# Performance work log

Hardware: AMD Instinct MI355X
Metric: run time of the kernel (lower is better)

## Reference

```python
import jax, jax.numpy as jnp
import numpy as np

B, S, HD, HE = 32, 2048, 1024, 1024

def setup_inputs() -> dict:
    key = jax.random.key(0)
    k1, k2, k3, k4, k5, k6 = jax.random.split(key, 6)
    decoder_hidden = jax.random.normal(k1, (B, HD), dtype=jnp.float32)
    encoder_outputs = jax.random.normal(k2, (B, S, HE), dtype=jnp.float32)
    src_mask = jax.random.randint(k3, (B, S), 0, 2) > 0
    # nn.Linear weights stored as [out, in]; apply as x @ W.T
    s_q = 1.0 / np.sqrt(HD)
    s_k = 1.0 / np.sqrt(HE)
    W_query = jax.random.uniform(k4, (HD, HD), jnp.float32, -s_q, s_q)
    W_key = jax.random.uniform(k5, (HD, HE), jnp.float32, -s_k, s_k)
    W_energy = jax.random.uniform(k6, (1, HD), jnp.float32, -s_q, s_q)
    return {
        "decoder_hidden": decoder_hidden,
        "encoder_outputs": encoder_outputs,
        "src_mask": src_mask,
        "W_query": W_query,
        "W_key": W_key,
        "W_energy": W_energy,
    }

def reference(decoder_hidden, encoder_outputs, src_mask, W_query, W_key, W_energy):
    # q: [B, 1, HD], k: [B, S, HD]
    q = (decoder_hidden @ W_query.T)[:, None, :]
    k = jnp.einsum("bse,de->bsd", encoder_outputs, W_key)
    # scores: [B, S] = v^T tanh(q + k)
    scores = jnp.einsum("bsd,d->bs", jnp.tanh(q + k), W_energy[0])
    scores = jnp.where(src_mask, scores, -1e9)
    attn_weights = jax.nn.softmax(scores, axis=-1)
    context = jnp.einsum("bs,bse->be", attn_weights, encoder_outputs)
    return context, attn_weights
```

## Files before the change

### kernel.cpp

```cpp
#include <hip/hip_runtime.h>
#include <hip/hip_bf16.h>


#define NB 32
#define SS 2048
#define HD 1024
#define HE 1024
#define MM (NB * SS)
#define NT 32

typedef float f32x4 __attribute__((ext_vector_type(4)));
typedef short bf16x8 __attribute__((ext_vector_type(8)));
typedef short short4v __attribute__((ext_vector_type(4)));

static __device__ __forceinline__ short f2bf(float f) {
    union { __hip_bfloat16 h; short s; } u;
    u.h = __float2bfloat16(f);
    return u.s;
}
static __device__ __forceinline__ float bf2f(short s) {
    union { float f; unsigned u; } u;
    u.u = ((unsigned)(unsigned short)s) << 16;
    return u.f;
}

static __device__ __forceinline__ void gload16(const void* g, const void* l) {
    __builtin_amdgcn_global_load_lds(
        (const __attribute__((address_space(1))) void*)(uintptr_t)(g),
        (__attribute__((address_space(3))) void*)(unsigned)(uintptr_t)(l),
        16, 0, 0);
}

__global__ __launch_bounds__(256) void prep_kernel(const int* __restrict__ mask,
                                                   const float* __restrict__ dh,
                                                   const float* __restrict__ Wq,
                                                   const float* __restrict__ Wk,
                                                   int* __restrict__ idx,
                                                   int* __restrict__ cnt,
                                                   float* __restrict__ q,
                                                   short* __restrict__ wkb) {
    const int bid  = blockIdx.x;
    const int tid  = threadIdx.x;
    const int wid  = tid >> 6;
    const int lane = tid & 63;

    if (bid < 8) {
        const int b = bid * 4 + wid;
        int base = 0;
        for (int s0 = 0; s0 < SS; s0 += 64) {
            const int m = mask[b * SS + s0 + lane];
            const unsigned long long bal = __ballot(m != 0);
            const int rank = __popcll(bal & ((1ull << lane) - 1ull));
            if (m) idx[b * SS + base + rank] = s0 + lane;
            base += (int)__popcll(bal);
        }
        if (lane == 0) cnt[b] = base;
        for (int j = base + lane; j < SS; j += 64) idx[b * SS + j] = 0;
    } else if (bid < 264) {
        const int d = (bid - 8) * 4 + wid;
        const float* wrow = Wq + (long)d * HD + lane * 16;
        f32x4 w0 = *(const f32x4*)(wrow + 0);
        f32x4 w1 = *(const f32x4*)(wrow + 4);
        f32x4 w2 = *(const f32x4*)(wrow + 8);
        f32x4 w3 = *(const f32x4*)(wrow + 12);
        for (int b = 0; b < NB; ++b) {
            const float* drow = dh + b * HD + lane * 16;
            f32x4 d0 = *(const f32x4*)(drow + 0);
            f32x4 d1 = *(const f32x4*)(drow + 4);
            f32x4 d2 = *(const f32x4*)(drow + 8);
            f32x4 d3 = *(const f32x4*)(drow + 12);
            f32x4 s4 = w0 * d0 + w1 * d1 + w2 * d2 + w3 * d3;
            float dot = s4[0] + s4[1] + s4[2] + s4[3];
            #pragma unroll
            for (int off = 32; off > 0; off >>= 1)
                dot += __shfl_xor(dot, off, 64);
            if (lane == 0) q[b * HD + d] = dot;
        }
    } else {
        const int i = (bid - 264) * 256 + tid;
        const f32x4 a = *(const f32x4*)(Wk + (long)i * 8);
        const f32x4 b = *(const f32x4*)(Wk + (long)i * 8 + 4);
        bf16x8 o;
        o[0] = f2bf(a[0]); o[1] = f2bf(a[1]); o[2] = f2bf(a[2]); o[3] = f2bf(a[3]);
        o[4] = f2bf(b[0]); o[5] = f2bf(b[1]); o[6] = f2bf(b[2]); o[7] = f2bf(b[3]);
        *(bf16x8*)(wkb + (long)i * 8) = o;
    }
}

__global__ __launch_bounds__(256) void cvt_enc_kernel(const float* __restrict__ enc,
                                                      const int* __restrict__ idx,
                                                      const int* __restrict__ cnt,
                                                      short* __restrict__ encb) {
    const int b  = blockIdx.x >> 7;
    const int j0 = (blockIdx.x & 127) * 16;
    const int n  = cnt[b];
    const int nr = (n + 127) & ~127;
    if (j0 >= nr) return;
    const int j  = j0 + (threadIdx.x >> 4);
    const int c0 = (threadIdx.x & 15) * 8;
    short* dst = encb + ((long)b * SS + j) * HE + c0;
    if (j < n) {
        const float* src = enc + ((long)b * SS + idx[b * SS + j]) * HE + c0;
        #pragma unroll
        for (int u = 0; u < 8; ++u) {
            const f32x4 x = *(const f32x4*)(src + u * 128);
            const f32x4 y = *(const f32x4*)(src + u * 128 + 4);
            bf16x8 o;
            o[0] = f2bf(x[0]); o[1] = f2bf(x[1]); o[2] = f2bf(x[2]); o[3] = f2bf(x[3]);
            o[4] = f2bf(y[0]); o[5] = f2bf(y[1]); o[6] = f2bf(y[2]); o[7] = f2bf(y[3]);
            *(bf16x8*)(dst + u * 128) = o;
        }
    } else {
        const bf16x8 z = (bf16x8){0,0,0,0,0,0,0,0};
        #pragma unroll
        for (int u = 0; u < 8; ++u) *(bf16x8*)(dst + u * 128) = z;
    }
}

__global__ __launch_bounds__(256, 3) void score_mfma_kernel(const short* __restrict__ encb,
                                                            const short* __restrict__ wkb,
                                                            const float* __restrict__ qv,
                                                            const float* __restrict__ ven,
                                                            const int* __restrict__ cnt,
                                                            float* __restrict__ sp) {
    __shared__ __align__(16) short As[2][4096];
    __shared__ __align__(16) short Bs[2][4096];

    const int bid   = blockIdx.x;
    const int xcd   = bid & 7;
    const int slot  = bid >> 3;
    const int mtile = xcd * 64 + (slot >> 3);
    const int nt    = slot & 7;

    const int bb   = mtile >> 4;
    const int tile = mtile & 15;
    if (tile * 128 >= cnt[bb]) return;

    const int tid  = threadIdx.x;
    const int lane = tid & 63;
    const int wid  = tid >> 6;
    const int wr   = wid >> 1;
    const int wc   = wid & 1;
    const long mbase = (long)bb * SS + tile * 128;
    const int  nbase = nt * 128;

    f32x4 acc[4][4];
    #pragma unroll
    for (int m = 0; m < 4; ++m)
        #pragma unroll
        for (int n = 0; n < 4; ++n)
            acc[m][n] = (f32x4){0.f, 0.f, 0.f, 0.f};

    const short* ag0 = encb + (mbase + (tid >> 2)) * (long)HE + (tid & 3) * 8;
    const short* ag1 = ag0 + 64 * (long)HE;
    const short* bg0 = wkb + ((long)(nbase + (tid >> 2))) * HE + (tid & 3) * 8;
    const short* bg1 = bg0 + 64 * (long)HE;

    const int frow = lane & 15;
    const int kby  = (lane >> 4) * 16;

    #define COMPUTE(BUF)                                                         \
        do {                                                                     \
            bf16x8 af[4], bfr[4];                                                \
            _Pragma("unroll")                                                    \
            for (int m = 0; m < 4; ++m)                                          \
                af[m] = *(const bf16x8*)((const char*)As[BUF]                    \
                          + (wr * 64 + m * 16 + frow) * 64 + kby);               \
            _Pragma("unroll")                                                    \
            for (int n = 0; n < 4; ++n)                                          \
                bfr[n] = *(const bf16x8*)((const char*)Bs[BUF]                   \
                          + (wc * 64 + n * 16 + frow) * 64 + kby);               \
            _Pragma("unroll")                                                    \
            for (int m = 0; m < 4; ++m)                                          \
                _Pragma("unroll")                                                \
                for (int n = 0; n < 4; ++n)                                      \
                    acc[m][n] = __builtin_amdgcn_mfma_f32_16x16x32_bf16(         \
                        af[m], bfr[n], acc[m][n], 0, 0, 0);                      \
        } while (0)

    for (int kt = 0; kt < NT; kt += 2) {
        const int ko0 = kt * 32;
        const int ko1 = ko0 + 32;
        gload16(ag0 + ko0, (char*)As[0] + wid * 1024);
        gload16(ag1 + ko0, (char*)As[0] + 4096 + wid * 1024);
        gload16(bg0 + ko0, (char*)Bs[0] + wid * 1024);
        gload16(bg1 + ko0, (char*)Bs[0] + 4096 + wid * 1024);
        gload16(ag0 + ko1, (char*)As[1] + wid * 1024);
        gload16(ag1 + ko1, (char*)As[1] + 4096 + wid * 1024);
        gload16(bg0 + ko1, (char*)Bs[1] + wid * 1024);
        gload16(bg1 + ko1, (char*)Bs[1] + 4096 + wid * 1024);
        __syncthreads();
        COMPUTE(0);
        COMPUTE(1);
        __syncthreads();
    }
    #undef COMPUTE

    float qq[4], vv[4];
    #pragma unroll
    for (int n = 0; n < 4; ++n) {
        const int c = nbase + wc * 64 + n * 16 + frow;
        qq[n] = qv[bb * HD + c];
        vv[n] = ven[c];
    }
    float p[4][4];
    #pragma unroll
    for (int m = 0; m < 4; ++m) {
        #pragma unroll
        for (int rg = 0; rg < 4; ++rg) {
            float s = 0.f;
            #pragma unroll
            for (int n = 0; n < 4; ++n) {
                const float x = acc[m][n][rg] + qq[n];
                const float e = __expf(2.f * x);
                const float t = 1.f - 2.f * __builtin_amdgcn_rcpf(e + 1.f);
                s += vv[n] * t;
            }
            #pragma unroll
            for (int msk = 1; msk <= 8; msk <<= 1)
                s += __shfl_xor(s, msk, 64);
            p[m][rg] = s;
        }
    }
    if ((lane & 15) == 0) {
        const int g = lane >> 4;
        float* dst = sp + (long)(nt * 2 + wc) * MM;
        #pragma unroll
        for (int m = 0; m < 4; ++m)
            #pragma unroll
            for (int rg = 0; rg < 4; ++rg)
                dst[mbase + wr * 64 + m * 16 + g * 4 + rg] = p[m][rg];
    }
}

__global__ __launch_bounds__(256) void softmax_kernel(const float* __restrict__ sp,
                                                      const int* __restrict__ idx,
                                                      const int* __restrict__ cnt,
                                                      float* __restrict__ attn,
                                                      float* __restrict__ wcomp) {
    const int b = blockIdx.x;
    const int tid = threadIdx.x;
    const int lane = tid & 63;
    const int wid = tid >> 6;
    const int n = cnt[b];
    #pragma unroll
    for (int i = 0; i < 8; ++i)
        attn[b * SS + tid + i * 256] = 0.f;
    __shared__ float red[4];
    float sc[8];
    float mx = -3.0e38f;
    #pragma unroll
    for (int i = 0; i < 8; ++i) {
        const int j = tid + i * 256;
        float v = -3.0e38f;
        if (j < n) {
            v = 0.f;
            #pragma unroll
            for (int k = 0; k < 16; ++k)
                v += sp[(long)k * MM + b * SS + j];
        }
        sc[i] = v;
        mx = fmaxf(mx, v);
    }
    #pragma unroll
    for (int off = 32; off > 0; off >>= 1)
        mx = fmaxf(mx, __shfl_xor(mx, off, 64));
    if (lane == 0) red[wid] = mx;
    __syncthreads();
    mx = fmaxf(fmaxf(red[0], red[1]), fmaxf(red[2], red[3]));
    __syncthreads();
    float sum = 0.f;
    #pragma unroll
    for (int i = 0; i < 8; ++i) {
        const float e = (sc[i] > -1.0e38f) ? __expf(sc[i] - mx) : 0.f;
        sc[i] = e;
        sum += e;
    }
    #pragma unroll
    for (int off = 32; off > 0; off >>= 1)
        sum += __shfl_xor(sum, off, 64);
    if (lane == 0) red[wid] = sum;
    __syncthreads();
    sum = red[0] + red[1] + red[2] + red[3];
    const float inv = 1.f / sum;
    #pragma unroll
    for (int i = 0; i < 8; ++i) {
        const int j = tid + i * 256;
        const float w = sc[i] * inv;
        wcomp[b * SS + j] = w;
        if (j < n) attn[b * SS + idx[b * SS + j]] = w;
    }
}

__global__ __launch_bounds__(256) void ctx_partial_kernel(const short* __restrict__ encb,
                                                          const float* __restrict__ wcomp,
                                                          const int* __restrict__ cnt,
                                                          float* __restrict__ cp) {
    const int b = blockIdx.x >> 5;
    const int chunk = blockIdx.x & 31;
    const int tid = threadIdx.x;
    float* dst = cp + ((long)(b * 32 + chunk)) * HE + tid * 4;
    if (chunk * 64 >= cnt[b]) {
        *(f32x4*)dst = (f32x4){0.f, 0.f, 0.f, 0.f};
        return;
    }
    const short* ep = encb + ((long)b * SS + chunk * 64) * HE + tid * 4;
    const float* ap = wcomp + b * SS + chunk * 64;
    f32x4 acc = (f32x4){0.f, 0.f, 0.f, 0.f};
    #pragma unroll 4
    for (int s = 0; s < 64; ++s) {
        const float w = ap[s];
        const short4v v = *(const short4v*)(ep + (long)s * HE);
        acc[0] += w * bf2f(v[0]);
        acc[1] += w * bf2f(v[1]);
        acc[2] += w * bf2f(v[2]);
        acc[3] += w * bf2f(v[3]);
    }
    *(f32x4*)dst = acc;
}

__global__ __launch_bounds__(256) void ctx_reduce_kernel(const float* __restrict__ cp,
                                                         float* __restrict__ out) {
    const int o = blockIdx.x * 256 + threadIdx.x;
    const int b = o >> 10;
    const int e = o & 1023;
    float s = 0.f;
    #pragma unroll
    for (int c = 0; c < 32; ++c)
        s += cp[((long)(b * 32 + c)) * HE + e];
    out[o] = s;
}

extern "C" void kernel_launch(void* const* d_in, const int* in_sizes, int n_in,
                              void* d_out, int out_size, void* d_ws, size_t ws_size,
                              hipStream_t stream) {
    const float* dh   = (const float*)d_in[0];
    const float* enc  = (const float*)d_in[1];
    const int*   mask = (const int*)d_in[2];
    const float* Wq   = (const float*)d_in[3];
    const float* Wk   = (const float*)d_in[4];
    const float* Ve   = (const float*)d_in[5];

    float* out  = (float*)d_out;
    float* ctx  = out;
    float* attn = out + NB * HD;

    float* ws    = (float*)d_ws;
    float* wq_   = ws;
    float* sp    = ws + 32768;
    float* cp    = sp + 16 * (long)MM;
    short* wkb   = (short*)(cp + 32 * 32 * HE);
    float* wcomp = (float*)(wkb + (long)HD * HE);
    int*   idx   = (int*)(wcomp + MM);
    int*   cnt   = idx + MM;
    short* encb  = (short*)(cnt + 64);

    prep_kernel<<<776, 256, 0, stream>>>(mask, dh, Wq, Wk, idx, cnt, wq_, wkb);
    cvt_enc_kernel<<<NB * 128, 256, 0, stream>>>(enc, idx, cnt, encb);
    score_mfma_kernel<<<4096, 256, 0, stream>>>(encb, wkb, wq_, Ve, cnt, sp);
    softmax_kernel<<<NB, 256, 0, stream>>>(sp, idx, cnt, attn, wcomp);
    ctx_partial_kernel<<<1024, 256, 0, stream>>>(encb, wcomp, cnt, cp);
    ctx_reduce_kernel<<<128, 256, 0, stream>>>(cp, ctx);
}
```

Before: 164.2 us.

## Double-buffer score GEMM LDS stages to overlap global loads with MFMA

Doubles the LDS staging buffers so the next K-chunk is prefetched via direct-to-LDS loads while the current chunk is computed. Manual s_waitcnt vmcnt(8) plus barriers replace the two __syncthreads per iteration. The goal is to hide global memory latency behind MFMA work. In exchange, LDS usage doubles to 64KB per block and the occupancy hint drops from 3 to 2 blocks per CU, which could reduce latency hiding across blocks.

Result: slower. 169.2 us (+3.1%).

```diff
diff --git a/kernel.cpp b/kernel.cpp
--- a/kernel.cpp
+++ b/kernel.cpp
@@ -117,14 +117,14 @@
     }
 }
 
-__global__ __launch_bounds__(256, 3) void score_mfma_kernel(const short* __restrict__ encb,
+__global__ __launch_bounds__(256, 2) void score_mfma_kernel(const short* __restrict__ encb,
                                                             const short* __restrict__ wkb,
                                                             const float* __restrict__ qv,
                                                             const float* __restrict__ ven,
                                                             const int* __restrict__ cnt,
                                                             float* __restrict__ sp) {
-    __shared__ __align__(16) short As[2][4096];
-    __shared__ __align__(16) short Bs[2][4096];
+    __shared__ __align__(16) short As[4 * 4096];
+    __shared__ __align__(16) short Bs[4 * 4096];
 
     const int bid   = blockIdx.x;
     const int xcd   = bid & 7;
@@ -159,16 +159,33 @@
     const int frow = lane & 15;
     const int kby  = (lane >> 4) * 16;
 
-    #define COMPUTE(BUF)                                                         \
+    #define ABASE(BUF, T) ((char*)As + ((BUF) * 2 + (T)) * 8192)
+    #define BBASE(BUF, T) ((char*)Bs + ((BUF) * 2 + (T)) * 8192)
+
+    #define STAGE(BUF, E)                                            \
+        do {                                                         \
+            const int ko0_ = (E) * 64;                               \
+            const int ko1_ = ko0_ + 32;                              \
+            gload16(ag0 + ko0_, ABASE(BUF, 0) + wid * 1024);         \
+            gload16(ag1 + ko0_, ABASE(BUF, 0) + 4096 + wid * 1024);  \
+            gload16(bg0 + ko0_, BBASE(BUF, 0) + wid * 1024);         \
+            gload16(bg1 + ko0_, BBASE(BUF, 0) + 4096 + wid * 1024);  \
+            gload16(ag0 + ko1_, ABASE(BUF, 1) + wid * 1024);         \
+            gload16(ag1 + ko1_, ABASE(BUF, 1) + 4096 + wid * 1024);  \
+            gload16(bg0 + ko1_, BBASE(BUF, 1) + wid * 1024);         \
+            gload16(bg1 + ko1_, BBASE(BUF, 1) + 4096 + wid * 1024);  \
+        } while (0)
+
+    #define COMPUTE(BUF, T)                                                      \
         do {                                                                     \
             bf16x8 af[4], bfr[4];                                                \
             _Pragma("unroll")                                                    \
             for (int m = 0; m < 4; ++m)                                          \
-                af[m] = *(const bf16x8*)((const char*)As[BUF]                    \
+                af[m] = *(const bf16x8*)(ABASE(BUF, T)                           \
                           + (wr * 64 + m * 16 + frow) * 64 + kby);               \
             _Pragma("unroll")                                                    \
             for (int n = 0; n < 4; ++n)                                          \
-                bfr[n] = *(const bf16x8*)((const char*)Bs[BUF]                   \
+                bfr[n] = *(const bf16x8*)(BBASE(BUF, T)                          \
                           + (wc * 64 + n * 16 + frow) * 64 + kby);               \
             _Pragma("unroll")                                                    \
             for (int m = 0; m < 4; ++m)                                          \
@@ -178,23 +195,24 @@
                         af[m], bfr[n], acc[m][n], 0, 0, 0);                      \
         } while (0)
 
-    for (int kt = 0; kt < NT; kt += 2) {
-        const int ko0 = kt * 32;
-        const int ko1 = ko0 + 32;
-        gload16(ag0 + ko0, (char*)As[0] + wid * 1024);
-        gload16(ag1 + ko0, (char*)As[0] + 4096 + wid * 1024);
-        gload16(bg0 + ko0, (char*)Bs[0] + wid * 1024);
-        gload16(bg1 + ko0, (char*)Bs[0] + 4096 + wid * 1024);
-        gload16(ag0 + ko1, (char*)As[1] + wid * 1024);
-        gload16(ag1 + ko1, (char*)As[1] + 4096 + wid * 1024);
-        gload16(bg0 + ko1, (char*)Bs[1] + wid * 1024);
-        gload16(bg1 + ko1, (char*)Bs[1] + 4096 + wid * 1024);
-        __syncthreads();
-        COMPUTE(0);
-        COMPUTE(1);
-        __syncthreads();
+    STAGE(0, 0);
+
+    for (int e = 0; e < 16; ++e) {
+        const int cur = e & 1;
+        if (e < 15) {
+            STAGE(cur ^ 1, e + 1);
+            asm volatile("s_waitcnt vmcnt(8)\n\ts_barrier" ::: "memory");
+        } else {
+            asm volatile("s_waitcnt vmcnt(0)\n\ts_barrier" ::: "memory");
+        }
+        COMPUTE(cur, 0);
+        COMPUTE(cur, 1);
+        asm volatile("s_barrier" ::: "memory");
     }
     #undef COMPUTE
+    #undef STAGE
+    #undef ABASE
+    #undef BBASE
 
     float qq[4], vv[4];
     #pragma unroll
```
